# Optimization experiments

Measured on AMD Instinct MI355X. Metric: run time of the kernel, lower is better.

## Reference

```python
import jax, jax.numpy as jnp
import numpy as np

L, M, B = 32768, 8, 8192      # lines, max neighbors per line, blocks
LIN, BIN, H = 768, 768, 512   # line_in_dim, block_in_dim, hidden_size
NH, DH = 8, 512 // 8          # heads, head_dim
LN_EPS = 1e-5


def _ln(x, g, b):
    mu = jnp.mean(x, axis=-1, keepdims=True)
    var = jnp.mean(jnp.square(x - mu), axis=-1, keepdims=True)
    return (x - mu) * jax.lax.rsqrt(var + LN_EPS) * g + b


def setup_inputs() -> dict:
    key = jax.random.key(0)
    ks = jax.random.split(key, 12)
    w = lambda k, shape, fan: jax.random.normal(k, shape, jnp.float32) * (fan ** -0.5)
    return {
        'global_lines': jax.random.normal(ks[0], (L, LIN), jnp.float32),
        'block_reprs': jax.random.normal(ks[1], (B, BIN), jnp.float32),
        'Wq': w(ks[2], (H, LIN), LIN),            # q_proj (no bias)
        'Wkv': w(ks[3], (H, BIN), BIN),           # kv_proj (no bias)
        'qn_g': jnp.ones((H,), jnp.float32), 'qn_b': jnp.zeros((H,), jnp.float32),
        'kvn_g': jnp.ones((H,), jnp.float32), 'kvn_b': jnp.zeros((H,), jnp.float32),
        'in_proj_w': w(ks[4], (3 * H, H), H), 'in_proj_b': jnp.zeros((3 * H,), jnp.float32),
        'out_w': w(ks[5], (H, H), H), 'out_b': jnp.zeros((H,), jnp.float32),
        'p1_w': w(ks[6], (H, 2 * H), 2 * H), 'p1_b': jnp.zeros((H,), jnp.float32),
        'ln1_g': jnp.ones((H,), jnp.float32), 'ln1_b': jnp.zeros((H,), jnp.float32),
        'p2_w': w(ks[7], (H, H), H), 'p2_b': jnp.zeros((H,), jnp.float32),
        'ln2_g': jnp.ones((H,), jnp.float32), 'ln2_b': jnp.zeros((H,), jnp.float32),
        'head_w': w(ks[8], (1, H), H), 'head_b': jnp.zeros((1,), jnp.float32),
        'K_indices': jax.random.randint(ks[9], (L, M), 0, B, jnp.int32),
        'neighbor_counts': jnp.clip(jax.random.randint(ks[10], (L,), 0, M + 1, jnp.int32), 1, M),
    }


def reference(global_lines, block_reprs, Wq, Wkv, qn_g, qn_b, kvn_g, kvn_b,
              in_proj_w, in_proj_b, out_w, out_b,
              p1_w, p1_b, ln1_g, ln1_b, p2_w, p2_b, ln2_g, ln2_b,
              head_w, head_b, K_indices, neighbor_counts):
    # q = LN(q_proj(lines))                              [L, H]
    q = _ln(global_lines @ Wq.T, qn_g, qn_b)
    # gather neighbor block reprs, project, LN           [L, M, H]
    kv = _ln(block_reprs[K_indices] @ Wkv.T, kvn_g, kvn_b)
    pad = jnp.arange(M)[None, :] >= neighbor_counts[:, None]  # True = padded key

    # torch nn.MultiheadAttention with query length 1 per line
    wq_i, wk_i, wv_i = jnp.split(in_proj_w, 3, axis=0)
    bq_i, bk_i, bv_i = jnp.split(in_proj_b, 3, axis=0)
    qh = (q @ wq_i.T + bq_i).reshape(L, NH, DH)
    kh = (kv @ wk_i.T + bk_i).reshape(L, M, NH, DH)
    vh = (kv @ wv_i.T + bv_i).reshape(L, M, NH, DH)
    scores = jnp.einsum('lhd,lmhd->lhm', qh, kh) / np.float32(np.sqrt(DH))
    scores = jnp.where(pad[:, None, :], jnp.finfo(scores.dtype).min, scores)
    attn = jax.nn.softmax(scores, axis=-1)
    ctx = jnp.einsum('lhm,lmhd->lhd', attn, vh).reshape(L, H)
    attn_out = ctx @ out_w.T + out_b

    # line_proj: Linear(2H->H) + LN + GELU + residual(Linear + LN + GELU)
    x = jnp.concatenate([q, attn_out], axis=-1)
    x = jax.nn.gelu(_ln(x @ p1_w.T + p1_b, ln1_g, ln1_b), approximate=False)
    x = x + jax.nn.gelu(_ln(x @ p2_w.T + p2_b, ln2_g, ln2_b), approximate=False)
    logits = (x @ head_w.T + head_b)[:, 0]
    return jax.nn.sigmoid(logits)
```

## Files before the change

### kernel.cpp

```cpp
#include <hip/hip_runtime.h>
#include <math.h>


typedef unsigned short u16;
typedef unsigned int u32;
using bf16x8 = __attribute__((ext_vector_type(8))) __bf16;
using u16x8  = __attribute__((ext_vector_type(8))) u16;
using f32x4  = __attribute__((ext_vector_type(4))) float;

__device__ __forceinline__ u16 f2bf(float f) {
    u32 u = __builtin_bit_cast(u32, f);
    u32 r = u + 0x7fffu + ((u >> 16) & 1u);
    return (u16)(r >> 16);
}
__device__ __forceinline__ float bf2f(u16 h) {
    return __builtin_bit_cast(float, (u32)h << 16);
}
__device__ __forceinline__ float gelu_exact(float x) {
    return 0.5f * x * (1.0f + erff(x * 0.70710678118654752440f));
}

__device__ __forceinline__ float breduce1(float s0, float* sm) {
    #pragma unroll
    for (int off = 32; off > 0; off >>= 1) s0 += __shfl_down(s0, off);
    const int lane = threadIdx.x & 63, w = threadIdx.x >> 6;
    __syncthreads();
    if (lane == 0) sm[w] = s0;
    __syncthreads();
    return sm[0] + sm[1] + sm[2] + sm[3];
}

struct CvtJobs {
    const float* s[5];
    u16* d[5];
    int cum[6];
};
__global__ __launch_bounds__(256) void cvt_multi(CvtJobs j)
{
    const int g = blockIdx.x * 256 + threadIdx.x;
    if (g >= j.cum[5]) return;
    int seg = 0;
    #pragma unroll
    for (int k = 1; k < 5; ++k) seg += (g >= j.cum[k]);
    const int q = g - j.cum[seg];
    const float4 v = *reinterpret_cast<const float4*>(j.s[seg] + q * 4);
    ushort4 o = make_ushort4(f2bf(v.x), f2bf(v.y), f2bf(v.z), f2bf(v.w));
    *reinterpret_cast<ushort4*>(j.d[seg] + q * 4) = o;
}

__global__ __launch_bounds__(256) void fold_w2(
    const float* __restrict__ p1w, const float* __restrict__ outw,
    u16* __restrict__ p1cb)
{
    __shared__ float As[16][65];
    __shared__ float Bs[16][65];
    const int tx = threadIdx.x & 15, ty = threadIdx.x >> 4;
    const int i0 = blockIdx.y * 64, j0 = blockIdx.x * 64;
    const int lr = threadIdx.x >> 2;
    const int lc = (threadIdx.x & 3) * 4;
    const int kr = threadIdx.x >> 4;
    const int jc = (threadIdx.x & 15) * 4;
    float acc[4][4] = {};
    for (int k0 = 0; k0 < 512; k0 += 16) {
        const float4 av = *reinterpret_cast<const float4*>(
            p1w + (size_t)(i0 + lr) * 1024 + 512 + k0 + lc);
        As[lc + 0][lr] = av.x; As[lc + 1][lr] = av.y;
        As[lc + 2][lr] = av.z; As[lc + 3][lr] = av.w;
        const float4 bv = *reinterpret_cast<const float4*>(
            outw + (size_t)(k0 + kr) * 512 + j0 + jc);
        Bs[kr][jc + 0] = bv.x; Bs[kr][jc + 1] = bv.y;
        Bs[kr][jc + 2] = bv.z; Bs[kr][jc + 3] = bv.w;
        __syncthreads();
        #pragma unroll
        for (int kk = 0; kk < 16; ++kk) {
            float a[4], b[4];
            #pragma unroll
            for (int i = 0; i < 4; ++i) a[i] = As[kk][ty * 4 + i];
            #pragma unroll
            for (int jj = 0; jj < 4; ++jj) b[jj] = Bs[kk][tx * 4 + jj];
            #pragma unroll
            for (int i = 0; i < 4; ++i)
                #pragma unroll
                for (int jj = 0; jj < 4; ++jj)
                    acc[i][jj] = fmaf(a[i], b[jj], acc[i][jj]);
        }
        __syncthreads();
    }
    #pragma unroll
    for (int i = 0; i < 4; ++i)
        #pragma unroll
        for (int jj = 0; jj < 4; ++jj)
            p1cb[(size_t)(i0 + ty * 4 + i) * 1024 + 512 + j0 + tx * 4 + jj] =
                f2bf(acc[i][jj]);
}

__global__ __launch_bounds__(64) void fold_bias(
    const float* __restrict__ p1w, const float* __restrict__ outb,
    const float* __restrict__ p1b, float* __restrict__ bias2)
{
    const int i = blockIdx.x, lane = threadIdx.x;
    float s = 0.0f;
    #pragma unroll
    for (int k = lane; k < 512; k += 64)
        s += p1w[(size_t)i * 1024 + 512 + k] * outb[k];
    #pragma unroll
    for (int off = 32; off > 0; off >>= 1) s += __shfl_down(s, off);
    if (lane == 0) bias2[i] = s + p1b[i];
}

template<int A_MODE, bool STATS>
__global__ __launch_bounds__(256) void gemm_bf16(
    const void* __restrict__ A1v, const void* __restrict__ A2v, int K1, int K,
    const u16* __restrict__ W, const float* __restrict__ bias,
    u16* __restrict__ C, int N, float* __restrict__ stats)
{
    __shared__ __bf16 As[2 * 128 * 32];
    __shared__ __bf16 Ws[2 * 128 * 32];
    const int tid = threadIdx.x;
    const int w = tid >> 6, lane = tid & 63;

    const u32 nx = gridDim.x;
    const u32 orig = blockIdx.y * nx + blockIdx.x;
    const u32 nwg = nx * gridDim.y;
    const u32 wgid = (orig & 7u) * (nwg >> 3) + (orig >> 3);
    const int bx = wgid % nx;
    const int row0 = (int)(wgid / nx) * 128;
    const int col0 = bx * 128;

    const int wr = (w >> 1) * 64, wc = (w & 1) * 64;
    const int fr = lane & 15, fg = lane >> 4;

    int srow[2], scol[2], soff[2];
    #pragma unroll
    for (int c = 0; c < 2; ++c) {
        const int bo = w * 2048 + c * 1024 + lane * 16;
        srow[c] = bo >> 6;
        scol[c] = (bo & 63) >> 1;
        soff[c] = (w * 2048 + c * 1024) >> 1;
    }
    const int ar = tid >> 1;
    const int ac = (tid & 1) * 16;

    f32x4 acc[4][4] = {};
    float4 av0, av1, av2, av3;

    auto stage_issue = [&](int k0, int buf) {
        if (A_MODE == 1) {
            const float* src = (const float*)A1v + (size_t)(row0 + ar) * K + k0 + ac;
            av0 = *reinterpret_cast<const float4*>(src);
            av1 = *reinterpret_cast<const float4*>(src + 4);
            av2 = *reinterpret_cast<const float4*>(src + 8);
            av3 = *reinterpret_cast<const float4*>(src + 12);
        } else {
            #pragma unroll
            for (int c = 0; c < 2; ++c) {
                const u16* asrc;
                if (A_MODE == 2) {
                    const bool first = (k0 < K1);
                    const u16* base = first ? (const u16*)A1v : (const u16*)A2v;
                    const int ldk = first ? K1 : (K - K1);
                    const int kk  = first ? k0 : (k0 - K1);
                    asrc = base + (size_t)(row0 + srow[c]) * ldk + kk + scol[c];
                } else {
                    asrc = (const u16*)A1v + (size_t)(row0 + srow[c]) * K + k0 + scol[c];
                }
                __builtin_amdgcn_global_load_lds(
                    (const __attribute__((address_space(1))) u32*)asrc,
                    (__attribute__((address_space(3))) u32*)(As + buf * 4096 + soff[c]),
                    16, 0, 0);
            }
        }
        #pragma unroll
        for (int c = 0; c < 2; ++c) {
            const u16* wsrc = W + (size_t)(col0 + srow[c]) * K + k0 + scol[c];
            __builtin_amdgcn_global_load_lds(
                (const __attribute__((address_space(1))) u32*)wsrc,
                (__attribute__((address_space(3))) u32*)(Ws + buf * 4096 + soff[c]),
                16, 0, 0);
        }
    };
    auto stage_write_a = [&](int buf) {
        u16x8 p0, p1;
        p0[0] = f2bf(av0.x); p0[1] = f2bf(av0.y); p0[2] = f2bf(av0.z); p0[3] = f2bf(av0.w);
        p0[4] = f2bf(av1.x); p0[5] = f2bf(av1.y); p0[6] = f2bf(av1.z); p0[7] = f2bf(av1.w);
        p1[0] = f2bf(av2.x); p1[1] = f2bf(av2.y); p1[2] = f2bf(av2.z); p1[3] = f2bf(av2.w);
        p1[4] = f2bf(av3.x); p1[5] = f2bf(av3.y); p1[6] = f2bf(av3.z); p1[7] = f2bf(av3.w);
        *reinterpret_cast<u16x8*>((u16*)As + buf * 4096 + ar * 32 + ac) = p0;
        *reinterpret_cast<u16x8*>((u16*)As + buf * 4096 + ar * 32 + ac + 8) = p1;
    };

    const int NT = K >> 5;
    int cur = 0;

    stage_issue(0, 0);
    if (A_MODE == 1) stage_write_a(0);
    __syncthreads();

    for (int t = 0; t < NT; ++t) {
        const bool have_next = (t + 1 < NT);
        if (have_next) stage_issue((t + 1) << 5, cur ^ 1);

        bf16x8 af[4], bfr[4];
        #pragma unroll
        for (int m = 0; m < 4; ++m) {
            af[m]  = *(const bf16x8*)(As + cur * 4096 + (wr + m * 16 + fr) * 32 + fg * 8);
            bfr[m] = *(const bf16x8*)(Ws + cur * 4096 + (wc + m * 16 + fr) * 32 + fg * 8);
        }
        #pragma unroll
        for (int m = 0; m < 4; ++m)
            #pragma unroll
            for (int n = 0; n < 4; ++n)
                acc[m][n] = __builtin_amdgcn_mfma_f32_16x16x32_bf16(
                    af[m], bfr[n], acc[m][n], 0, 0, 0);

        if (have_next && A_MODE == 1) stage_write_a(cur ^ 1);
        __syncthreads();
        cur ^= 1;
    }

    if (bias) {
        #pragma unroll
        for (int n = 0; n < 4; ++n) {
            const float bv = bias[col0 + wc + n * 16 + fr];
            #pragma unroll
            for (int m = 0; m < 4; ++m)
                #pragma unroll
                for (int r = 0; r < 4; ++r)
                    acc[m][n][r] += bv;
        }
    }

    #pragma unroll
    for (int m = 0; m < 4; ++m)
        #pragma unroll
        for (int n = 0; n < 4; ++n) {
            const int col = col0 + wc + n * 16 + fr;
            #pragma unroll
            for (int r = 0; r < 4; ++r) {
                const int row = row0 + wr + m * 16 + fg * 4 + r;
                C[(size_t)row * N + col] = f2bf(acc[m][n][r]);
            }
        }

    if (STATS) {
        float ps[4][4], pq[4][4];
        #pragma unroll
        for (int m = 0; m < 4; ++m)
            #pragma unroll
            for (int r = 0; r < 4; ++r) {
                float s = 0.0f, q2 = 0.0f;
                #pragma unroll
                for (int n = 0; n < 4; ++n) {
                    const float v = acc[m][n][r];
                    s += v; q2 = fmaf(v, v, q2);
                }
                ps[m][r] = s; pq[m][r] = q2;
            }
        #pragma unroll
        for (int off = 1; off < 16; off <<= 1)
            #pragma unroll
            for (int m = 0; m < 4; ++m)
                #pragma unroll
                for (int r = 0; r < 4; ++r) {
                    ps[m][r] += __shfl_xor(ps[m][r], off);
                    pq[m][r] += __shfl_xor(pq[m][r], off);
                }
        if (fr == 0) {
            const int cb = bx * 2 + (w & 1);
            #pragma unroll
            for (int m = 0; m < 4; ++m)
                #pragma unroll
                for (int r = 0; r < 4; ++r) {
                    const int row = row0 + wr + m * 16 + fg * 4 + r;
                    *reinterpret_cast<float2*>(stats + ((size_t)row * 8 + cb) * 2) =
                        make_float2(ps[m][r], pq[m][r]);
                }
        }
    }
}

template<bool GELU>
__global__ __launch_bounds__(256) void ln_rows_s(
    u16* __restrict__ X, const float* __restrict__ stats,
    const float* __restrict__ g, const float* __restrict__ b)
{
    const size_t row = blockIdx.x;
    float s = 0.0f, q2 = 0.0f;
    #pragma unroll
    for (int cb = 0; cb < 8; ++cb) {
        s  += stats[(row * 8 + cb) * 2];
        q2 += stats[(row * 8 + cb) * 2 + 1];
    }
    const float mu = s * (1.0f / 512.0f);
    const float var = q2 * (1.0f / 512.0f) - mu * mu;
    const float rs = rsqrtf(var + 1e-5f);
    const int t = threadIdx.x;
    const ushort2 xv = *reinterpret_cast<const ushort2*>(X + row * 512 + 2 * t);
    const float2 gg = *reinterpret_cast<const float2*>(g + 2 * t);
    const float2 bb = *reinterpret_cast<const float2*>(b + 2 * t);
    float y0 = (bf2f(xv.x) - mu) * rs * gg.x + bb.x;
    float y1 = (bf2f(xv.y) - mu) * rs * gg.y + bb.y;
    if (GELU) { y0 = gelu_exact(y0); y1 = gelu_exact(y1); }
    *reinterpret_cast<ushort2*>(X + row * 512 + 2 * t) = make_ushort2(f2bf(y0), f2bf(y1));
}

__global__ __launch_bounds__(512) void attn_kernel(
    const u16* __restrict__ qh, const u16* __restrict__ kvb,
    const int* __restrict__ kidx, const int* __restrict__ ncnt,
    u16* __restrict__ ctx)
{
    const int head = threadIdx.x >> 6;
    const int lane = threadIdx.x & 63;
    const int mi = lane & 7, dg = lane >> 3;
    const bool b0 = (mi & 1), b1 = (mi & 2), b2 = (mi & 4);
    const int doff = (b0 ? 4 : 0) + (b1 ? 2 : 0) + (b2 ? 1 : 0);

    for (int l = blockIdx.x; l < 32768; l += gridDim.x) {
        const int cnt = ncnt[l];
        const int idx = kidx[l * 8 + mi];
        const size_t kvbase = (size_t)idx * 1024 + head * 64 + dg * 8;

        const u16x8 qv = *(const u16x8*)(qh + (size_t)l * 512 + head * 64 + dg * 8);
        const u16x8 kv = *(const u16x8*)(kvb + kvbase);
        const u16x8 vv = *(const u16x8*)(kvb + kvbase + 512);

        float p = 0.0f;
        #pragma unroll
        for (int jj = 0; jj < 8; ++jj) p = fmaf(bf2f(qv[jj]), bf2f(kv[jj]), p);
        p += __shfl_xor(p, 8); p += __shfl_xor(p, 16); p += __shfl_xor(p, 32);

        float s = (mi < cnt) ? p * 0.125f : -3.402823466e38f;
        float mx = s;
        mx = fmaxf(mx, __shfl_xor(mx, 1));
        mx = fmaxf(mx, __shfl_xor(mx, 2));
        mx = fmaxf(mx, __shfl_xor(mx, 4));
        const float e = __expf(s - mx);
        float den = e;
        den += __shfl_xor(den, 1); den += __shfl_xor(den, 2); den += __shfl_xor(den, 4);
        const float wgt = e / den;

        float c[8];
        #pragma unroll
        for (int jj = 0; jj < 8; ++jj) c[jj] = wgt * bf2f(vv[jj]);

        #pragma unroll
        for (int jj = 0; jj < 4; ++jj) {
            const float snd = b0 ? c[jj] : c[jj + 4];
            const float rec = __shfl_xor(snd, 1);
            c[jj] = (b0 ? c[jj + 4] : c[jj]) + rec;
        }
        #pragma unroll
        for (int jj = 0; jj < 2; ++jj) {
            const float snd = b1 ? c[jj] : c[jj + 2];
            const float rec = __shfl_xor(snd, 2);
            c[jj] = (b1 ? c[jj + 2] : c[jj]) + rec;
        }
        {
            const float snd = b2 ? c[0] : c[1];
            const float rec = __shfl_xor(snd, 4);
            c[0] = (b2 ? c[1] : c[0]) + rec;
        }
        ctx[(size_t)l * 512 + head * 64 + dg * 8 + doff] = f2bf(c[0]);
    }
}

__global__ __launch_bounds__(256) void final_head_s(
    const u16* __restrict__ h1, const u16* __restrict__ h2raw,
    const float* __restrict__ stats,
    const float* __restrict__ g, const float* __restrict__ b,
    const float* __restrict__ hw, const float* __restrict__ hb,
    float* __restrict__ out)
{
    __shared__ float sm[4];
    const size_t row = blockIdx.x;
    float s = 0.0f, q2 = 0.0f;
    #pragma unroll
    for (int cb = 0; cb < 8; ++cb) {
        s  += stats[(row * 8 + cb) * 2];
        q2 += stats[(row * 8 + cb) * 2 + 1];
    }
    const float mu = s * (1.0f / 512.0f);
    const float var = q2 * (1.0f / 512.0f) - mu * mu;
    const float rs = rsqrtf(var + 1e-5f);
    const int t = threadIdx.x;
    const ushort2 xv = *reinterpret_cast<const ushort2*>(h2raw + row * 512 + 2 * t);
    const ushort2 hv = *reinterpret_cast<const ushort2*>(h1 + row * 512 + 2 * t);
    const float2 gg = *reinterpret_cast<const float2*>(g + 2 * t);
    const float2 bb = *reinterpret_cast<const float2*>(b + 2 * t);
    const float2 hwv = *reinterpret_cast<const float2*>(hw + 2 * t);
    const float y0 = bf2f(hv.x) + gelu_exact((bf2f(xv.x) - mu) * rs * gg.x + bb.x);
    const float y1 = bf2f(hv.y) + gelu_exact((bf2f(xv.y) - mu) * rs * gg.y + bb.y);
    const float d = breduce1(y0 * hwv.x + y1 * hwv.y, sm);
    if (t == 0) out[row] = 1.0f / (1.0f + expf(-(d + hb[0])));
}

extern "C" void kernel_launch(void* const* d_in, const int* in_sizes, int n_in,
                              void* d_out, int out_size, void* d_ws, size_t ws_size,
                              hipStream_t stream)
{
    const float* lines  = (const float*)d_in[0];
    const float* blocks = (const float*)d_in[1];
    const float* Wq     = (const float*)d_in[2];
    const float* Wkv    = (const float*)d_in[3];
    const float* qn_g   = (const float*)d_in[4];
    const float* qn_b   = (const float*)d_in[5];
    const float* kvn_g  = (const float*)d_in[6];
    const float* kvn_b  = (const float*)d_in[7];
    const float* in_w   = (const float*)d_in[8];
    const float* in_b   = (const float*)d_in[9];
    const float* out_w  = (const float*)d_in[10];
    const float* out_b  = (const float*)d_in[11];
    const float* p1_w   = (const float*)d_in[12];
    const float* p1_b   = (const float*)d_in[13];
    const float* ln1_g  = (const float*)d_in[14];
    const float* ln1_b  = (const float*)d_in[15];
    const float* p2_w   = (const float*)d_in[16];
    const float* p2_b   = (const float*)d_in[17];
    const float* ln2_g  = (const float*)d_in[18];
    const float* ln2_b  = (const float*)d_in[19];
    const float* head_w = (const float*)d_in[20];
    const float* head_b = (const float*)d_in[21];
    const int*   kidx   = (const int*)d_in[22];
    const int*   ncnt   = (const int*)d_in[23];
    float* out = (float*)d_out;

    char* wsb = (char*)d_ws;
    u16* qb    = (u16*)(wsb);
    u16* qhb   = (u16*)(wsb + (32ull << 20));
    u16* ctxb  = (u16*)(wsb + (64ull << 20));
    u16* kvbb  = (u16*)(wsb + (96ull << 20));
    u16* bkvb  = (u16*)(wsb + (112ull << 20));
    float* stats_q   = (float*)(wsb + (120ull << 20));
    float* stats_h1  = (float*)(wsb + (124ull << 20));
    float* stats_h2  = (float*)(wsb + (128ull << 20));
    float* stats_bkv = (float*)(wsb + (132ull << 20));
    u16* Wqb   = (u16*)(wsb + (136ull << 20));
    u16* Wkvb  = Wqb + 512 * 768;
    u16* inwb  = Wkvb + 512 * 768;
    u16* p1cb  = inwb + 1536 * 512;
    u16* p2wb  = p1cb + 512 * 1024;
    float* bias2f = (float*)(p2wb + 512 * 512);

    {
        CvtJobs j;
        const float* ss[5] = { Wq, Wkv, in_w, p1_w, p2_w };
        u16* dd[5] = { Wqb, Wkvb, inwb, p1cb, p2wb };
        const int nn[5] = { 512 * 768, 512 * 768, 1536 * 512, 512 * 1024, 512 * 512 };
        int c = 0;
        for (int k = 0; k < 5; ++k) { j.s[k] = ss[k]; j.d[k] = dd[k]; j.cum[k] = c; c += nn[k] / 4; }
        j.cum[5] = c;
        cvt_multi<<<(c + 255) / 256, 256, 0, stream>>>(j);
    }
    fold_w2<<<dim3(8, 8), 256, 0, stream>>>(p1_w, out_w, p1cb);
    fold_bias<<<512, 64, 0, stream>>>(p1_w, out_b, p1_b, bias2f);

    gemm_bf16<1, true><<<dim3(4, 64), 256, 0, stream>>>(
        blocks, nullptr, 768, 768, Wkvb, nullptr, bkvb, 512, stats_bkv);
    ln_rows_s<false><<<8192, 256, 0, stream>>>(bkvb, stats_bkv, kvn_g, kvn_b);
    gemm_bf16<0, false><<<dim3(8, 64), 256, 0, stream>>>(
        bkvb, nullptr, 512, 512, inwb + 512 * 512, in_b + 512, kvbb, 1024, nullptr);
    gemm_bf16<1, true><<<dim3(4, 256), 256, 0, stream>>>(
        lines, nullptr, 768, 768, Wqb, nullptr, qb, 512, stats_q);
    ln_rows_s<false><<<32768, 256, 0, stream>>>(qb, stats_q, qn_g, qn_b);
    gemm_bf16<0, false><<<dim3(4, 256), 256, 0, stream>>>(
        qb, nullptr, 512, 512, inwb, in_b, qhb, 512, nullptr);
    attn_kernel<<<2048, 512, 0, stream>>>(qhb, kvbb, kidx, ncnt, ctxb);
    gemm_bf16<2, true><<<dim3(4, 256), 256, 0, stream>>>(
        qb, ctxb, 512, 1024, p1cb, bias2f, qhb, 512, stats_h1);
    ln_rows_s<true><<<32768, 256, 0, stream>>>(qhb, stats_h1, ln1_g, ln1_b);
    gemm_bf16<0, true><<<dim3(4, 256), 256, 0, stream>>>(
        qhb, nullptr, 512, 512, p2wb, p2_b, ctxb, 512, stats_h2);
    final_head_s<<<32768, 256, 0, stream>>>(qhb, ctxb, stats_h2, ln2_g, ln2_b,
                                            head_w, head_b, out);
}
```

Baseline: 449.5 us.

## Fuse LayerNorm/GELU prologues into GEMM A-loading and drop standalone LN kernels

Removes the separate ln_rows_s passes. Each consumer GEMM now loads the raw bf16 activations plus per-row statistics, and applies LayerNorm (and GELU where needed) while staging A into LDS. The final head kernel recomputes LN1+GELU from the raw h1 and its stats instead of reading a normalized buffer. This avoids four read-modify-write passes over large activation tensors. In exchange, normalization is recomputed in every column block, which multiplies the GELU/erf work, and A loads go through registers instead of direct global-to-LDS loads.

```diff
diff --git a/kernel.cpp b/kernel.cpp
--- a/kernel.cpp
+++ b/kernel.cpp
@@ -108,9 +108,11 @@
     if (lane == 0) bias2[i] = s + p1b[i];
 }
 
-template<int A_MODE, bool STATS>
+template<int A_MODE, bool STATS, bool AGELU>
 __global__ __launch_bounds__(256) void gemm_bf16(
-    const void* __restrict__ A1v, const void* __restrict__ A2v, int K1, int K,
+    const void* __restrict__ A1v, const void* __restrict__ A2v,
+    const float* __restrict__ statsA, const float* __restrict__ gA,
+    const float* __restrict__ bA, int K1, int K,
     const u16* __restrict__ W, const float* __restrict__ bias,
     u16* __restrict__ C, int N, float* __restrict__ stats)
 {
@@ -141,8 +143,22 @@
     const int ar = tid >> 1;
     const int ac = (tid & 1) * 16;
 
+    float mu = 0.0f, rs = 0.0f;
+    if (A_MODE >= 2) {
+        float s = 0.0f, q2 = 0.0f;
+        #pragma unroll
+        for (int cb = 0; cb < 8; ++cb) {
+            const float2 t2 = *reinterpret_cast<const float2*>(
+                statsA + ((size_t)(row0 + ar) * 8 + cb) * 2);
+            s += t2.x; q2 += t2.y;
+        }
+        mu = s * (1.0f / 512.0f);
+        rs = rsqrtf(q2 * (1.0f / 512.0f) - mu * mu + 1e-5f);
+    }
+
     f32x4 acc[4][4] = {};
     float4 av0, av1, av2, av3;
+    u16x8 xr0, xr1;
 
     auto stage_issue = [&](int k0, int buf) {
         if (A_MODE == 1) {
@@ -151,16 +167,18 @@
             av1 = *reinterpret_cast<const float4*>(src + 4);
             av2 = *reinterpret_cast<const float4*>(src + 8);
             av3 = *reinterpret_cast<const float4*>(src + 12);
+        } else if (A_MODE == 3 || (A_MODE == 2 && k0 < K1)) {
+            const int ld = (A_MODE == 2) ? K1 : K;
+            const u16* src = (const u16*)A1v + (size_t)(row0 + ar) * ld + k0 + ac;
+            xr0 = *reinterpret_cast<const u16x8*>(src);
+            xr1 = *reinterpret_cast<const u16x8*>(src + 8);
         } else {
             #pragma unroll
             for (int c = 0; c < 2; ++c) {
                 const u16* asrc;
                 if (A_MODE == 2) {
-                    const bool first = (k0 < K1);
-                    const u16* base = first ? (const u16*)A1v : (const u16*)A2v;
-                    const int ldk = first ? K1 : (K - K1);
-                    const int kk  = first ? k0 : (k0 - K1);
-                    asrc = base + (size_t)(row0 + srow[c]) * ldk + kk + scol[c];
+                    asrc = (const u16*)A2v +
+                           (size_t)(row0 + srow[c]) * (K - K1) + (k0 - K1) + scol[c];
                 } else {
                     asrc = (const u16*)A1v + (size_t)(row0 + srow[c]) * K + k0 + scol[c];
                 }
@@ -179,26 +197,53 @@
                 16, 0, 0);
         }
     };
-    auto stage_write_a = [&](int buf) {
-        u16x8 p0, p1;
-        p0[0] = f2bf(av0.x); p0[1] = f2bf(av0.y); p0[2] = f2bf(av0.z); p0[3] = f2bf(av0.w);
-        p0[4] = f2bf(av1.x); p0[5] = f2bf(av1.y); p0[6] = f2bf(av1.z); p0[7] = f2bf(av1.w);
-        p1[0] = f2bf(av2.x); p1[1] = f2bf(av2.y); p1[2] = f2bf(av2.z); p1[3] = f2bf(av2.w);
-        p1[4] = f2bf(av3.x); p1[5] = f2bf(av3.y); p1[6] = f2bf(av3.z); p1[7] = f2bf(av3.w);
-        *reinterpret_cast<u16x8*>((u16*)As + buf * 4096 + ar * 32 + ac) = p0;
-        *reinterpret_cast<u16x8*>((u16*)As + buf * 4096 + ar * 32 + ac + 8) = p1;
+    auto stage_write = [&](int k0, int buf) {
+        if (A_MODE == 0) return;
+        if (A_MODE == 2 && k0 >= K1) return;
+        u16x8 o0, o1;
+        if (A_MODE == 1) {
+            o0[0] = f2bf(av0.x); o0[1] = f2bf(av0.y); o0[2] = f2bf(av0.z); o0[3] = f2bf(av0.w);
+            o0[4] = f2bf(av1.x); o0[5] = f2bf(av1.y); o0[6] = f2bf(av1.z); o0[7] = f2bf(av1.w);
+            o1[0] = f2bf(av2.x); o1[1] = f2bf(av2.y); o1[2] = f2bf(av2.z); o1[3] = f2bf(av2.w);
+            o1[4] = f2bf(av3.x); o1[5] = f2bf(av3.y); o1[6] = f2bf(av3.z); o1[7] = f2bf(av3.w);
+        } else {
+            float gv[16], bv[16];
+            *reinterpret_cast<float4*>(&gv[0])  = *(const float4*)(gA + k0 + ac);
+            *reinterpret_cast<float4*>(&gv[4])  = *(const float4*)(gA + k0 + ac + 4);
+            *reinterpret_cast<float4*>(&gv[8])  = *(const float4*)(gA + k0 + ac + 8);
+            *reinterpret_cast<float4*>(&gv[12]) = *(const float4*)(gA + k0 + ac + 12);
+            *reinterpret_cast<float4*>(&bv[0])  = *(const float4*)(bA + k0 + ac);
+            *reinterpret_cast<float4*>(&bv[4])  = *(const float4*)(bA + k0 + ac + 4);
+            *reinterpret_cast<float4*>(&bv[8])  = *(const float4*)(bA + k0 + ac + 8);
+            *reinterpret_cast<float4*>(&bv[12]) = *(const float4*)(bA + k0 + ac + 12);
+            #pragma unroll
+            for (int jj = 0; jj < 8; ++jj) {
+                float y = (bf2f((u16)xr0[jj]) - mu) * rs * gv[jj] + bv[jj];
+                if (AGELU) y = gelu_exact(y);
+                o0[jj] = f2bf(y);
+            }
+            #pragma unroll
+            for (int jj = 0; jj < 8; ++jj) {
+                float y = (bf2f((u16)xr1[jj]) - mu) * rs * gv[jj + 8] + bv[jj + 8];
+                if (AGELU) y = gelu_exact(y);
+                o1[jj] = f2bf(y);
+            }
+        }
+        *reinterpret_cast<u16x8*>((u16*)As + buf * 4096 + ar * 32 + ac) = o0;
+        *reinterpret_cast<u16x8*>((u16*)As + buf * 4096 + ar * 32 + ac + 8) = o1;
     };
 
     const int NT = K >> 5;
     int cur = 0;
 
     stage_issue(0, 0);
-    if (A_MODE == 1) stage_write_a(0);
+    stage_write(0, 0);
     __syncthreads();
 
     for (int t = 0; t < NT; ++t) {
-        const bool have_next = (t + 1 < NT);
-        if (have_next) stage_issue((t + 1) << 5, cur ^ 1);
+        const int k0n = (t + 1) << 5;
+        const bool hn = (t + 1 < NT);
+        if (hn) stage_issue(k0n, cur ^ 1);
 
         bf16x8 af[4], bfr[4];
         #pragma unroll
@@ -213,7 +258,7 @@
                 acc[m][n] = __builtin_amdgcn_mfma_f32_16x16x32_bf16(
                     af[m], bfr[n], acc[m][n], 0, 0, 0);
 
-        if (have_next && A_MODE == 1) stage_write_a(cur ^ 1);
+        if (hn) stage_write(k0n, cur ^ 1);
         __syncthreads();
         cur ^= 1;
     }
@@ -221,12 +266,12 @@
     if (bias) {
         #pragma unroll
         for (int n = 0; n < 4; ++n) {
-            const float bv = bias[col0 + wc + n * 16 + fr];
+            const float bvv = bias[col0 + wc + n * 16 + fr];
             #pragma unroll
             for (int m = 0; m < 4; ++m)
                 #pragma unroll
                 for (int r = 0; r < 4; ++r)
-                    acc[m][n][r] += bv;
+                    acc[m][n][r] += bvv;
         }
     }
 
@@ -279,31 +324,6 @@
     }
 }
 
-template<bool GELU>
-__global__ __launch_bounds__(256) void ln_rows_s(
-    u16* __restrict__ X, const float* __restrict__ stats,
-    const float* __restrict__ g, const float* __restrict__ b)
-{
-    const size_t row = blockIdx.x;
-    float s = 0.0f, q2 = 0.0f;
-    #pragma unroll
-    for (int cb = 0; cb < 8; ++cb) {
-        s  += stats[(row * 8 + cb) * 2];
-        q2 += stats[(row * 8 + cb) * 2 + 1];
-    }
-    const float mu = s * (1.0f / 512.0f);
-    const float var = q2 * (1.0f / 512.0f) - mu * mu;
-    const float rs = rsqrtf(var + 1e-5f);
-    const int t = threadIdx.x;
-    const ushort2 xv = *reinterpret_cast<const ushort2*>(X + row * 512 + 2 * t);
-    const float2 gg = *reinterpret_cast<const float2*>(g + 2 * t);
-    const float2 bb = *reinterpret_cast<const float2*>(b + 2 * t);
-    float y0 = (bf2f(xv.x) - mu) * rs * gg.x + bb.x;
-    float y1 = (bf2f(xv.y) - mu) * rs * gg.y + bb.y;
-    if (GELU) { y0 = gelu_exact(y0); y1 = gelu_exact(y1); }
-    *reinterpret_cast<ushort2*>(X + row * 512 + 2 * t) = make_ushort2(f2bf(y0), f2bf(y1));
-}
-
 __global__ __launch_bounds__(512) void attn_kernel(
     const u16* __restrict__ qh, const u16* __restrict__ kvb,
     const int* __restrict__ kidx, const int* __restrict__ ncnt,
@@ -365,31 +385,38 @@
 }
 
 __global__ __launch_bounds__(256) void final_head_s(
-    const u16* __restrict__ h1, const u16* __restrict__ h2raw,
-    const float* __restrict__ stats,
-    const float* __restrict__ g, const float* __restrict__ b,
+    const u16* __restrict__ h1raw, const u16* __restrict__ h2raw,
+    const float* __restrict__ st1, const float* __restrict__ st2,
+    const float* __restrict__ g1, const float* __restrict__ b1,
+    const float* __restrict__ g2, const float* __restrict__ b2,
     const float* __restrict__ hw, const float* __restrict__ hb,
     float* __restrict__ out)
 {
     __shared__ float sm[4];
     const size_t row = blockIdx.x;
-    float s = 0.0f, q2 = 0.0f;
+    float s1 = 0.0f, q1 = 0.0f, s2 = 0.0f, q2 = 0.0f;
     #pragma unroll
     for (int cb = 0; cb < 8; ++cb) {
-        s  += stats[(row * 8 + cb) * 2];
-        q2 += stats[(row * 8 + cb) * 2 + 1];
-    }
-    const float mu = s * (1.0f / 512.0f);
-    const float var = q2 * (1.0f / 512.0f) - mu * mu;
-    const float rs = rsqrtf(var + 1e-5f);
+        const float2 a = *reinterpret_cast<const float2*>(st1 + (row * 8 + cb) * 2);
+        const float2 c = *reinterpret_cast<const float2*>(st2 + (row * 8 + cb) * 2);
+        s1 += a.x; q1 += a.y; s2 += c.x; q2 += c.y;
+    }
+    const float mu1 = s1 * (1.0f / 512.0f);
+    const float rs1 = rsqrtf(q1 * (1.0f / 512.0f) - mu1 * mu1 + 1e-5f);
+    const float mu2 = s2 * (1.0f / 512.0f);
+    const float rs2 = rsqrtf(q2 * (1.0f / 512.0f) - mu2 * mu2 + 1e-5f);
     const int t = threadIdx.x;
-    const ushort2 xv = *reinterpret_cast<const ushort2*>(h2raw + row * 512 + 2 * t);
-    const ushort2 hv = *reinterpret_cast<const ushort2*>(h1 + row * 512 + 2 * t);
-    const float2 gg = *reinterpret_cast<const float2*>(g + 2 * t);
-    const float2 bb = *reinterpret_cast<const float2*>(b + 2 * t);
+    const ushort2 x1 = *reinterpret_cast<const ushort2*>(h1raw + row * 512 + 2 * t);
+    const ushort2 x2 = *reinterpret_cast<const ushort2*>(h2raw + row * 512 + 2 * t);
+    const float2 g1v = *reinterpret_cast<const float2*>(g1 + 2 * t);
+    const float2 b1v = *reinterpret_cast<const float2*>(b1 + 2 * t);
+    const float2 g2v = *reinterpret_cast<const float2*>(g2 + 2 * t);
+    const float2 b2v = *reinterpret_cast<const float2*>(b2 + 2 * t);
     const float2 hwv = *reinterpret_cast<const float2*>(hw + 2 * t);
-    const float y0 = bf2f(hv.x) + gelu_exact((bf2f(xv.x) - mu) * rs * gg.x + bb.x);
-    const float y1 = bf2f(hv.y) + gelu_exact((bf2f(xv.y) - mu) * rs * gg.y + bb.y);
+    const float y0 = gelu_exact((bf2f(x1.x) - mu1) * rs1 * g1v.x + b1v.x)
+                   + gelu_exact((bf2f(x2.x) - mu2) * rs2 * g2v.x + b2v.x);
+    const float y1 = gelu_exact((bf2f(x1.y) - mu1) * rs1 * g1v.y + b1v.y)
+                   + gelu_exact((bf2f(x2.y) - mu2) * rs2 * g2v.y + b2v.y);
     const float d = breduce1(y0 * hwv.x + y1 * hwv.y, sm);
     if (t == 0) out[row] = 1.0f / (1.0f + expf(-(d + hb[0])));
 }
@@ -454,22 +481,26 @@
     fold_w2<<<dim3(8, 8), 256, 0, stream>>>(p1_w, out_w, p1cb);
     fold_bias<<<512, 64, 0, stream>>>(p1_w, out_b, p1_b, bias2f);
 
-    gemm_bf16<1, true><<<dim3(4, 64), 256, 0, stream>>>(
-        blocks, nullptr, 768, 768, Wkvb, nullptr, bkvb, 512, stats_bkv);
-    ln_rows_s<false><<<8192, 256, 0, stream>>>(bkvb, stats_bkv, kvn_g, kvn_b);
-    gemm_bf16<0, false><<<dim3(8, 64), 256, 0, stream>>>(
-        bkvb, nullptr, 512, 512, inwb + 512 * 512, in_b + 512, kvbb, 1024, nullptr);
-    gemm_bf16<1, true><<<dim3(4, 256), 256, 0, stream>>>(
-        lines, nullptr, 768, 768, Wqb, nullptr, qb, 512, stats_q);
-    ln_rows_s<false><<<32768, 256, 0, stream>>>(qb, stats_q, qn_g, qn_b);
-    gemm_bf16<0, false><<<dim3(4, 256), 256, 0, stream>>>(
-        qb, nullptr, 512, 512, inwb, in_b, qhb, 512, nullptr);
+    gemm_bf16<1, true, false><<<dim3(4, 64), 256, 0, stream>>>(
+        blocks, nullptr, nullptr, nullptr, nullptr, 768, 768,
+        Wkvb, nullptr, bkvb, 512, stats_bkv);
+    gemm_bf16<3, false, false><<<dim3(8, 64), 256, 0, stream>>>(
+        bkvb, nullptr, stats_bkv, kvn_g, kvn_b, 512, 512,
+        inwb + 512 * 512, in_b + 512, kvbb, 1024, nullptr);
+    gemm_bf16<1, true, false><<<dim3(4, 256), 256, 0, stream>>>(
+        lines, nullptr, nullptr, nullptr, nullptr, 768, 768,
+        Wqb, nullptr, qb, 512, stats_q);
+    gemm_bf16<3, false, false><<<dim3(4, 256), 256, 0, stream>>>(
+        qb, nullptr, stats_q, qn_g, qn_b, 512, 512,
+        inwb, in_b, qhb, 512, nullptr);
     attn_kernel<<<2048, 512, 0, stream>>>(qhb, kvbb, kidx, ncnt, ctxb);
-    gemm_bf16<2, true><<<dim3(4, 256), 256, 0, stream>>>(
-        qb, ctxb, 512, 1024, p1cb, bias2f, qhb, 512, stats_h1);
-    ln_rows_s<true><<<32768, 256, 0, stream>>>(qhb, stats_h1, ln1_g, ln1_b);
-    gemm_bf16<0, true><<<dim3(4, 256), 256, 0, stream>>>(
-        qhb, nullptr, 512, 512, p2wb, p2_b, ctxb, 512, stats_h2);
-    final_head_s<<<32768, 256, 0, stream>>>(qhb, ctxb, stats_h2, ln2_g, ln2_b,
+    gemm_bf16<2, true, false><<<dim3(4, 256), 256, 0, stream>>>(
+        qb, ctxb, stats_q, qn_g, qn_b, 512, 1024,
+        p1cb, bias2f, qhb, 512, stats_h1);
+    gemm_bf16<3, true, true><<<dim3(4, 256), 256, 0, stream>>>(
+        qhb, nullptr, stats_h1, ln1_g, ln1_b, 512, 512,
+        p2wb, p2_b, ctxb, 512, stats_h2);
+    final_head_s<<<32768, 256, 0, stream>>>(qhb, ctxb, stats_h1, stats_h2,
+                                            ln1_g, ln1_b, ln2_g, ln2_b,
                                             head_w, head_b, out);
 }
```

After: 523.7 us. 1.16x slower.
